# Kernel optimization log

Hardware: AMD Instinct MI355X
Metric: run time of the kernel (lower is better)

Reference implementation:

```python
import jax, jax.numpy as jnp
import numpy as np
from jax.scipy.special import logsumexp

EPS_SINK = 0.1
N_ITERS = 100
LN_EPS = 1e-5
ANAT_W = (1.0, 1.0, 1.2)  # anatomical_weights[0:3] used by _get_region_weights
GRIDS = ((5, 0.2), (15, 0.3), (25, 0.5))  # (grid_size, scale_weight)


def layernorm(x, g, b):
    m = x.mean(-1, keepdims=True)
    v = ((x - m) ** 2).mean(-1, keepdims=True)
    return (x - m) / jnp.sqrt(v + LN_EPS) * g + b


def spatial_distribution(bb, g):
    # bb: [B, D, 4] in 0..1000 coords -> [B, D, g*g] binary occupancy grid
    B, D, _ = bb.shape
    bc = bb * (g / 1000.0)
    x, y, w, h = bc[..., 0], bc[..., 1], bc[..., 2], bc[..., 3]
    x1 = jnp.maximum(jnp.trunc(x), 0.0)          # max(0, int(x))
    y1 = jnp.maximum(jnp.trunc(y), 0.0)
    x2 = jnp.minimum(jnp.trunc(x + w), g - 1.0)  # min(g-1, int(x+w))
    y2 = jnp.minimum(jnp.trunc(y + h), g - 1.0)
    gi = jnp.arange(g, dtype=bb.dtype)
    row = (gi[None, None, :, None] >= y1[..., None, None]) & (gi[None, None, :, None] <= y2[..., None, None])
    col = (gi[None, None, None, :] >= x1[..., None, None]) & (gi[None, None, None, :] <= x2[..., None, None])
    nz = jnp.any(bc != 0, axis=-1)[..., None, None]
    grid = (row & col & nz).astype(bb.dtype)  # [B, D, g, g]
    return grid.reshape(B, D, g * g)


def emd_pairs(d1, d2, g):
    # d1, d2: [B, P, n] spatial distributions; returns [B, P] pseudo-EMD exactly as source
    yy, xx = jnp.meshgrid(jnp.arange(g), jnp.arange(g), indexing='ij')
    pos = jnp.stack([xx.ravel(), yy.ravel()], axis=1).astype(jnp.float32)
    diff = pos[:, None, :] - pos[None, :, :]
    C = jnp.sqrt((diff * diff).sum(-1))
    C = C / C.max()
    rw = jnp.ones((g, g), jnp.float32)
    rw = rw.at[: g // 3].mul(ANAT_W[0]).at[g // 3 : (2 * g) // 3].mul(ANAT_W[1]).at[(2 * g) // 3 :].mul(ANAT_W[2])
    C = C * rw.ravel()  # broadcast over columns, same as torch C[n,n] * weights[n]
    K = jnp.exp(-C / EPS_SINK)
    logP = jnp.log(d1[..., :, None] + 1e-8)  # [B,P,n,1]
    logQ = jnp.log(d2[..., None, :] + 1e-8)  # [B,P,1,n]

    def step(carry, _):
        u, v = carry
        u = logP - logsumexp(v + K, axis=-1, keepdims=True)
        v = logQ - logsumexp(u + K.T, axis=-2, keepdims=True)
        return (u, v), None

    (u, v), _ = jax.lax.scan(step, (jnp.zeros_like(logP), jnp.zeros_like(logQ)), None, length=N_ITERS)
    Pm = jnp.exp(u + v + K)
    return (Pm * C).sum((-2, -1))


def setup_inputs() -> dict:
    key = jax.random.key(0)
    ks = jax.random.split(key, 6)
    B, D, F, Hd = 1, 14, 768, 256
    features = jax.random.normal(ks[0], (B, D, F), jnp.float32)
    # x,y in [0,800), w,h in [0,200) so boxes stay inside the 0..1000 frame
    bb = jax.random.uniform(ks[1], (B, D, 4), jnp.float32) * jnp.array([800.0, 800.0, 200.0, 200.0])
    return {
        'features': features,
        'bb_coords': bb,
        'w_embed': jax.random.normal(ks[2], (F, Hd), jnp.float32) * 0.02,
        'b_embed': jnp.zeros((Hd,), jnp.float32),
        'g1': jnp.ones((Hd,), jnp.float32),
        'b1': jnp.zeros((Hd,), jnp.float32),
        'gat_W': jax.random.normal(ks[3], (3, Hd, Hd), jnp.float32) * 0.02,
        'gat_b': jnp.zeros((3, Hd), jnp.float32),
        'gat_g': jnp.ones((3, Hd), jnp.float32),
        'gat_bt': jnp.zeros((3, Hd), jnp.float32),
        'w_out': jax.random.normal(ks[4], (Hd, F), jnp.float32) * 0.02,
        'b_out': jnp.zeros((F,), jnp.float32),
        'g2': jnp.ones((F,), jnp.float32),
        'b2': jnp.zeros((F,), jnp.float32),
    }


def reference(features, bb_coords, w_embed, b_embed, g1, b1, gat_W, gat_b, gat_g, gat_bt, w_out, b_out, g2, b2):
    B, D, _ = features.shape
    H = 1  # num_heads (the only shape-consistent value for the source module)
    x = layernorm(features @ w_embed + b_embed, g1, b1)

    # --- EMD-based adjacency over all 91 unordered disease pairs, vectorized ---
    iu, ju = np.triu_indices(D, k=1)
    adj = jnp.zeros((B, D, D), features.dtype)
    for g, sw in GRIDS:
        dist = spatial_distribution(bb_coords, g)            # [B, D, g*g]
        emd = emd_pairs(dist[:, iu], dist[:, ju], g)         # [B, 91]
        adj = adj.at[:, iu, ju].add(sw * emd).at[:, ju, iu].add(sw * emd)
    adj = jax.nn.softmax(adj, axis=-1)

    # --- 3 GAT layers (q=k=v, per source) ---
    attns = []
    for l in range(3):
        h = x @ gat_W[l] + gat_b[l]                          # [B, D, 256]
        hd = h.shape[-1] // H
        q = h.reshape(B, D, H, hd).transpose(0, 2, 1, 3)     # [B, H, D, hd]
        attn = jnp.einsum('bhnd,bhmd->bhnm', q, q) * hd ** -0.5
        attn = jnp.where(adj[:, None] == 0, -jnp.inf, attn)
        attn = jax.nn.softmax(attn, axis=-1)
        o = jnp.einsum('bhnm,bhmd->bhnd', attn, q)
        o = o.transpose(0, 2, 1, 3).reshape(B, D, H * hd)
        x = layernorm(o, gat_g[l], gat_bt[l])
        attns.append(attn.mean(1))
        x = jax.nn.elu(x)

    out = layernorm(x @ w_out + b_out, g2, b2)
    final_attention = jnp.stack(attns).mean(0)
    return out, final_attention
```

## Files before the change

### kernel.cpp

```cpp
#include <hip/hip_runtime.h>
#include <math.h>


#define NWG 16

__device__ __forceinline__ void astore(float* p, float v) {
  __hip_atomic_store(p, v, __ATOMIC_RELAXED, __HIP_MEMORY_SCOPE_AGENT);
}

__device__ __forceinline__ void bar_arrive(int* bar, int slot) {
  asm volatile("s_waitcnt vmcnt(0)" ::: "memory");
  __syncthreads();
  if (threadIdx.x == 0)
    __hip_atomic_fetch_add(&bar[slot], 1, __ATOMIC_RELAXED,
                           __HIP_MEMORY_SCOPE_AGENT);
}

__device__ __forceinline__ void bar_wait(int* bar, int slot) {
  if (threadIdx.x == 0) {
    while (__hip_atomic_load(&bar[slot], __ATOMIC_RELAXED,
                             __HIP_MEMORY_SCOPE_AGENT) < NWG)
      __builtin_amdgcn_s_sleep(1);
  }
  __syncthreads();
  asm volatile("" ::: "memory");
}

__device__ __forceinline__ float blockReduce512(float v, float* red) {
#pragma unroll
  for (int off = 32; off; off >>= 1) v += __shfl_xor(v, off);
  __syncthreads();
  if ((threadIdx.x & 63) == 0) red[threadIdx.x >> 6] = v;
  __syncthreads();
  return ((red[0] + red[1]) + (red[2] + red[3])) +
         ((red[4] + red[5]) + (red[6] + red[7]));
}

__device__ __forceinline__ void row_stats(const float* Xs, float* Pb,
                                          float* Mn, float* Rs, int tid) {
  if (tid < 224) {
    const int r = tid >> 4, seg = tid & 15;
    const float* p = Xs + r * 260 + seg * 16;
    const float4 a = *(const float4*)(p);
    const float4 b = *(const float4*)(p + 4);
    const float4 c = *(const float4*)(p + 8);
    const float4 d = *(const float4*)(p + 12);
    Pb[tid] = (((a.x + a.y) + (a.z + a.w)) + ((b.x + b.y) + (b.z + b.w))) +
              (((c.x + c.y) + (c.z + c.w)) + ((d.x + d.y) + (d.z + d.w)));
  }
  __syncthreads();
  if (tid < 14) {
    float s = 0.f;
#pragma unroll
    for (int q = 0; q < 16; ++q) s += Pb[tid * 16 + q];
    Mn[tid] = s * (1.f / 256.f);
  }
  __syncthreads();
  if (tid < 224) {
    const int r = tid >> 4, seg = tid & 15;
    const float m = Mn[r];
    const float* p = Xs + r * 260 + seg * 16;
    float s = 0.f;
#pragma unroll
    for (int i = 0; i < 16; ++i) {
      const float dv = p[i] - m;
      s = fmaf(dv, dv, s);
    }
    Pb[tid] = s;
  }
  __syncthreads();
  if (tid < 14) {
    float s = 0.f;
#pragma unroll
    for (int q = 0; q < 16; ++q) s += Pb[tid * 16 + q];
    Rs[tid] = rsqrtf(s * (1.f / 256.f) + 1e-5f);
  }
  __syncthreads();
}

__global__ __launch_bounds__(512) void sdg_fused(
    const float* __restrict__ feat, const float* __restrict__ w_embed,
    const float* __restrict__ b_embed, const float* __restrict__ g1,
    const float* __restrict__ b1, const float* __restrict__ gat_W,
    const float* __restrict__ gat_b, const float* __restrict__ gat_g,
    const float* __restrict__ gat_bt, const float* __restrict__ w_out,
    const float* __restrict__ b_out, const float* __restrict__ g2,
    const float* __restrict__ b2, float* __restrict__ out, int* bar,
    float* __restrict__ e_ws, float* __restrict__ h_ws,
    float* __restrict__ gp_ws, float* __restrict__ obuf) {
  const int w = blockIdx.x, tid = threadIdx.x;
  const int w16 = w * 16, w48 = w * 48;
  const int c = tid & 15, ks = tid >> 4;

  __shared__ __align__(16) float SA[13056];
  __shared__ __align__(16) float SB[10752];
  __shared__ __align__(16) float Pb[7200];
  __shared__ float Hb[240];
  __shared__ float Asm[224];
  __shared__ float aRow[224];
  __shared__ float Mn[14], Rs[14];
  __shared__ float red8[8];

  float* const Fs = SB;
  float* const Xs = SB;
  float* const Ht = SB + 3640;

#pragma unroll
  for (int i = 0; i < 6; ++i) {
    const int idx = i * 512 + tid;
    const int k = idx >> 2, q = (idx & 3) * 4;
    const float4 v = *(const float4*)(&w_embed[k * 256 + w16 + q]);
    SA[k * 17 + q + 0] = v.x;
    SA[k * 17 + q + 1] = v.y;
    SA[k * 17 + q + 2] = v.z;
    SA[k * 17 + q + 3] = v.w;
  }
  for (int i = tid; i < 2688; i += 512)
    *(float4*)(&Fs[i * 4]) = ((const float4*)feat)[i];
  if (tid < 224) aRow[tid] = 0.f;
  if (tid < 28) Asm[(tid >> 1) * 16 + 14 + (tid & 1)] = 0.f;
  __syncthreads();

  {
    float acc[14];
#pragma unroll
    for (int r = 0; r < 14; ++r) acc[r] = 0.f;
    const int kb = ks * 24;
#pragma unroll
    for (int ch = 0; ch < 6; ++ch) {
      const int k = kb + ch * 4;
      const float w0 = SA[(k + 0) * 17 + c];
      const float w1 = SA[(k + 1) * 17 + c];
      const float w2 = SA[(k + 2) * 17 + c];
      const float w3 = SA[(k + 3) * 17 + c];
#pragma unroll
      for (int r = 0; r < 14; ++r) {
        const float4 xv = *(const float4*)(&Fs[r * 768 + k]);
        acc[r] = fmaf(xv.x, w0,
                      fmaf(xv.y, w1, fmaf(xv.z, w2, fmaf(xv.w, w3, acc[r]))));
      }
    }
#pragma unroll
    for (int r = 0; r < 14; ++r) Pb[ks * 225 + r * 16 + c] = acc[r];
  }
  __syncthreads();
  if (tid < 224) {
    float v = b_embed[w16 + (tid & 15)];
#pragma unroll
    for (int q = 0; q < 32; ++q) v += Pb[q * 225 + tid];
    astore(&e_ws[(tid >> 4) * 256 + w16 + (tid & 15)], v);
  }
  bar_arrive(bar, 0);
#pragma unroll
  for (int i = 0; i < 2; ++i) {
    const int idx = i * 512 + tid;
    const int k = idx >> 2, q = (idx & 3) * 4;
    const float4 v = *(const float4*)(&gat_W[k * 256 + w16 + q]);
    SA[k * 17 + q + 0] = v.x;
    SA[k * 17 + q + 1] = v.y;
    SA[k * 17 + q + 2] = v.z;
    SA[k * 17 + q + 3] = v.w;
  }
  bar_wait(bar, 0);

  for (int i = tid; i < 896; i += 512) {
    const float4 v = ((const float4*)e_ws)[i];
    const int idx = i * 4, r = idx >> 8, cc = idx & 255;
    *(float4*)(&Xs[r * 260 + cc]) = v;
  }
  for (int i = tid; i < 520; i += 512) Ht[14 * 260 + i] = 0.f;
  __syncthreads();
  row_stats(Xs, Pb, Mn, Rs, tid);
  for (int i = tid; i < 3584; i += 512) {
    const int r = i >> 8, cc = i & 255;
    Xs[r * 260 + cc] = (Xs[r * 260 + cc] - Mn[r]) * Rs[r] * g1[cc] + b1[cc];
  }
  __syncthreads();

  for (int l = 0; l < 3; ++l) {
    {
      float acc[14];
#pragma unroll
      for (int r = 0; r < 14; ++r) acc[r] = 0.f;
      const int kb = ks * 8;
#pragma unroll
      for (int ch = 0; ch < 2; ++ch) {
        const int k = kb + ch * 4;
        const float w0 = SA[(k + 0) * 17 + c];
        const float w1 = SA[(k + 1) * 17 + c];
        const float w2 = SA[(k + 2) * 17 + c];
        const float w3 = SA[(k + 3) * 17 + c];
#pragma unroll
        for (int r = 0; r < 14; ++r) {
          const float4 xv = *(const float4*)(&Xs[r * 260 + k]);
          acc[r] = fmaf(
              xv.x, w0, fmaf(xv.y, w1, fmaf(xv.z, w2, fmaf(xv.w, w3, acc[r]))));
        }
      }
#pragma unroll
      for (int r = 0; r < 14; ++r) Pb[ks * 225 + r * 16 + c] = acc[r];
    }
    __syncthreads();
    if (tid < 224) {
      float v = gat_b[l * 256 + w16 + (tid & 15)];
#pragma unroll
      for (int q = 0; q < 32; ++q) v += Pb[q * 225 + tid];
      Hb[(tid >> 4) * 17 + (tid & 15)] = v;
      astore(&h_ws[l * 3584 + (tid >> 4) * 256 + w16 + (tid & 15)], v);
    }
    __syncthreads();
    if (tid < 196) {
      const int i = tid / 14, j = tid - i * 14;
      float s = 0.f;
#pragma unroll
      for (int cc = 0; cc < 16; ++cc)
        s = fmaf(Hb[i * 17 + cc], Hb[j * 17 + cc], s);
      astore(&gp_ws[l * 3328 + w * 208 + tid], s);
    }
    bar_arrive(bar, 1 + l);
    if (l < 2) {
      const float* Wn = gat_W + (l + 1) * 65536;
#pragma unroll
      for (int i = 0; i < 2; ++i) {
        const int idx = i * 512 + tid;
        const int k = idx >> 2, q = (idx & 3) * 4;
        const float4 v = *(const float4*)(&Wn[k * 256 + w16 + q]);
        SA[k * 17 + q + 0] = v.x;
        SA[k * 17 + q + 1] = v.y;
        SA[k * 17 + q + 2] = v.z;
        SA[k * 17 + q + 3] = v.w;
      }
    } else {
#pragma unroll
      for (int g = 0; g < 3; ++g)
#pragma unroll
        for (int i = 0; i < 2; ++i) {
          const int idx = i * 512 + tid;
          const int k = idx >> 2, q = (idx & 3) * 4;
          const float4 v = *(const float4*)(&w_out[k * 768 + w48 + g * 16 + q]);
          SA[g * 4352 + k * 17 + q + 0] = v.x;
          SA[g * 4352 + k * 17 + q + 1] = v.y;
          SA[g * 4352 + k * 17 + q + 2] = v.z;
          SA[g * 4352 + k * 17 + q + 3] = v.w;
        }
    }
    bar_wait(bar, 1 + l);

    float glog = 0.f;
    if (tid < 196) {
      const float* gpl = gp_ws + l * 3328 + tid;
#pragma unroll
      for (int ww = 0; ww < 16; ++ww) glog += gpl[ww * 208];
    }
    for (int i = tid; i < 896; i += 512) {
      const float4 v = ((const float4*)(h_ws + l * 3584))[i];
      const int idx = i * 4, r = idx >> 8, cc = idx & 255;
      *(float4*)(&Ht[r * 260 + cc]) = v;
    }
    if (tid < 196) {
      const int i = tid / 14, j = tid - i * 14;
      Asm[i * 16 + j] = glog * 0.0625f;
    }
    __syncthreads();
    if (tid < 224) {
      const int r = tid >> 4, j = tid & 15;
      const float lv = (j < 14) ? Asm[r * 16 + j] : -1e30f;
      float mx = lv;
#pragma unroll
      for (int off = 8; off; off >>= 1) mx = fmaxf(mx, __shfl_xor(mx, off, 16));
      float p = (j < 14) ? expf(lv - mx) : 0.f;
      float sm = p;
#pragma unroll
      for (int off = 8; off; off >>= 1) sm += __shfl_xor(sm, off, 16);
      p /= sm;
      if (j < 14) {
        Asm[r * 16 + j] = p;
        aRow[r * 16 + j] += p * (1.f / 3.f);
      }
    }
    __syncthreads();
    if (l == 2 && w < 14 && tid < 14)
      out[10752 + w * 14 + tid] = aRow[w * 16 + tid];
    const int half = tid >> 8, t2 = tid & 255;
    float o[7];
#pragma unroll
    for (int rr = 0; rr < 7; ++rr) o[rr] = 0.f;
#pragma unroll
    for (int mc = 0; mc < 4; ++mc) {
      const float v0 = Ht[(mc * 4 + 0) * 260 + t2];
      const float v1 = Ht[(mc * 4 + 1) * 260 + t2];
      const float v2 = Ht[(mc * 4 + 2) * 260 + t2];
      const float v3 = Ht[(mc * 4 + 3) * 260 + t2];
#pragma unroll
      for (int rr = 0; rr < 7; ++rr) {
        const float4 a = *(const float4*)(&Asm[(half * 7 + rr) * 16 + mc * 4]);
        o[rr] =
            fmaf(a.x, v0, fmaf(a.y, v1, fmaf(a.z, v2, fmaf(a.w, v3, o[rr]))));
      }
    }
#pragma unroll
    for (int rr = 0; rr < 7; ++rr) Xs[(half * 7 + rr) * 260 + t2] = o[rr];
    __syncthreads();
    row_stats(Xs, Pb, Mn, Rs, tid);
    {
      const float gc = gat_g[l * 256 + t2], bc = gat_bt[l * 256 + t2];
#pragma unroll
      for (int rr = 0; rr < 7; ++rr) {
        const int r = half * 7 + rr;
        const float xn = (o[rr] - Mn[r]) * Rs[r] * gc + bc;
        Xs[r * 260 + t2] = xn > 0.f ? xn : expm1f(xn);
      }
    }
    __syncthreads();
  }

  for (int g = 0; g < 3; ++g) {
    float acc[14];
#pragma unroll
    for (int r = 0; r < 14; ++r) acc[r] = 0.f;
    const int kb = ks * 8;
#pragma unroll
    for (int ch = 0; ch < 2; ++ch) {
      const int k = kb + ch * 4;
      const float w0 = SA[g * 4352 + (k + 0) * 17 + c];
      const float w1 = SA[g * 4352 + (k + 1) * 17 + c];
      const float w2 = SA[g * 4352 + (k + 2) * 17 + c];
      const float w3 = SA[g * 4352 + (k + 3) * 17 + c];
#pragma unroll
      for (int r = 0; r < 14; ++r) {
        const float4 xv = *(const float4*)(&Xs[r * 260 + k]);
        acc[r] = fmaf(
            xv.x, w0, fmaf(xv.y, w1, fmaf(xv.z, w2, fmaf(xv.w, w3, acc[r]))));
      }
    }
#pragma unroll
    for (int r = 0; r < 14; ++r) Pb[ks * 225 + r * 16 + c] = acc[r];
    __syncthreads();
    if (tid < 224) {
      float v = b_out[w48 + g * 16 + (tid & 15)];
#pragma unroll
      for (int q = 0; q < 32; ++q) v += Pb[q * 225 + tid];
      astore(&obuf[(tid >> 4) * 768 + w48 + g * 16 + (tid & 15)], v);
    }
    __syncthreads();
  }
  bar_arrive(bar, 4);
  bar_wait(bar, 4);

  if (w < 14) {
    const int d = w;
    const float a = obuf[d * 768 + tid];
    const float b = (tid < 256) ? obuf[d * 768 + 512 + tid] : 0.f;
    const float m = blockReduce512(a + b, red8) * (1.f / 768.f);
    const float da = a - m, db = b - m;
    const float var =
        blockReduce512(da * da + ((tid < 256) ? db * db : 0.f), red8) *
        (1.f / 768.f);
    const float rs = rsqrtf(var + 1e-5f);
    out[d * 768 + tid] = da * rs * g2[tid] + b2[tid];
    if (tid < 256)
      out[d * 768 + 512 + tid] = db * rs * g2[512 + tid] + b2[512 + tid];
  }
}

extern "C" void kernel_launch(void* const* d_in, const int* in_sizes, int n_in,
                              void* d_out, int out_size, void* d_ws,
                              size_t ws_size, hipStream_t stream) {
  const float* feat = (const float*)d_in[0];
  const float* w_embed = (const float*)d_in[2];
  const float* b_embed = (const float*)d_in[3];
  const float* g1 = (const float*)d_in[4];
  const float* b1 = (const float*)d_in[5];
  const float* gat_W = (const float*)d_in[6];
  const float* gat_b = (const float*)d_in[7];
  const float* gat_g = (const float*)d_in[8];
  const float* gat_bt = (const float*)d_in[9];
  const float* w_out = (const float*)d_in[10];
  const float* b_out = (const float*)d_in[11];
  const float* g2 = (const float*)d_in[12];
  const float* b2 = (const float*)d_in[13];
  float* out = (float*)d_out;

  int* bar = (int*)d_ws;
  float* e_ws = (float*)d_ws + 16;
  float* h_ws = e_ws + 3584;
  float* gp_ws = h_ws + 3 * 3584;
  float* obuf = gp_ws + 3 * 3328;

  hipMemsetAsync(bar, 0, 16 * sizeof(int), stream);
  sdg_fused<<<NWG, 512, 0, stream>>>(feat, w_embed, b_embed, g1, b1, gat_W,
                                     gat_b, gat_g, gat_bt, w_out, b_out, g2,
                                     b2, out, bar, e_ws, h_ws, gp_ws, obuf);
}
```

Baseline: 42.42 us.

## Double block size and compute layernorm stats via partial sums across workgroups

```diff
diff --git a/kernel.cpp b/kernel.cpp
--- a/kernel.cpp
+++ b/kernel.cpp
@@ -24,16 +24,6 @@
   }
   __syncthreads();
   asm volatile("" ::: "memory");
-}
-
-__device__ __forceinline__ float blockReduce512(float v, float* red) {
-#pragma unroll
-  for (int off = 32; off; off >>= 1) v += __shfl_xor(v, off);
-  __syncthreads();
-  if ((threadIdx.x & 63) == 0) red[threadIdx.x >> 6] = v;
-  __syncthreads();
-  return ((red[0] + red[1]) + (red[2] + red[3])) +
-         ((red[4] + red[5]) + (red[6] + red[7]));
 }
 
 __device__ __forceinline__ void row_stats(const float* Xs, float* Pb,
@@ -78,7 +68,7 @@
   __syncthreads();
 }
 
-__global__ __launch_bounds__(512) void sdg_fused(
+__global__ __launch_bounds__(1024) void sdg_fused(
     const float* __restrict__ feat, const float* __restrict__ w_embed,
     const float* __restrict__ b_embed, const float* __restrict__ g1,
     const float* __restrict__ b1, const float* __restrict__ gat_W,
@@ -87,91 +77,120 @@
     const float* __restrict__ b_out, const float* __restrict__ g2,
     const float* __restrict__ b2, float* __restrict__ out, int* bar,
     float* __restrict__ e_ws, float* __restrict__ h_ws,
-    float* __restrict__ gp_ws, float* __restrict__ obuf) {
+    float* __restrict__ gp_ws, float* __restrict__ st1_ws,
+    float* __restrict__ st2_ws) {
   const int w = blockIdx.x, tid = threadIdx.x;
   const int w16 = w * 16, w48 = w * 48;
-  const int c = tid & 15, ks = tid >> 4;
-
-  __shared__ __align__(16) float SA[13056];
+  const int c = tid & 15;
+  const int ksl = (tid >> 4) & 15;
+  const int rg = tid >> 8;
+
+  __shared__ __align__(16) float SA[14592];
   __shared__ __align__(16) float SB[10752];
-  __shared__ __align__(16) float Pb[7200];
+  __shared__ __align__(16) float Pb[3600];
   __shared__ float Hb[240];
   __shared__ float Asm[224];
   __shared__ float aRow[224];
-  __shared__ float Mn[14], Rs[14];
-  __shared__ float red8[8];
+  __shared__ float Ov[686];
+  __shared__ float Mn[14], Rs[14], ps[14], psq[14];
 
   float* const Fs = SB;
   float* const Xs = SB;
   float* const Ht = SB + 3640;
 
 #pragma unroll
-  for (int i = 0; i < 6; ++i) {
-    const int idx = i * 512 + tid;
+  for (int i = 0; i < 3; ++i) {
+    const int idx = i * 1024 + tid;
     const int k = idx >> 2, q = (idx & 3) * 4;
     const float4 v = *(const float4*)(&w_embed[k * 256 + w16 + q]);
-    SA[k * 17 + q + 0] = v.x;
-    SA[k * 17 + q + 1] = v.y;
-    SA[k * 17 + q + 2] = v.z;
-    SA[k * 17 + q + 3] = v.w;
-  }
-  for (int i = tid; i < 2688; i += 512)
+    SA[k * 19 + q + 0] = v.x;
+    SA[k * 19 + q + 1] = v.y;
+    SA[k * 19 + q + 2] = v.z;
+    SA[k * 19 + q + 3] = v.w;
+  }
+  for (int i = tid; i < 2688; i += 1024)
     *(float4*)(&Fs[i * 4]) = ((const float4*)feat)[i];
   if (tid < 224) aRow[tid] = 0.f;
   if (tid < 28) Asm[(tid >> 1) * 16 + 14 + (tid & 1)] = 0.f;
   __syncthreads();
 
   {
-    float acc[14];
-#pragma unroll
-    for (int r = 0; r < 14; ++r) acc[r] = 0.f;
-    const int kb = ks * 24;
-#pragma unroll
-    for (int ch = 0; ch < 6; ++ch) {
+    float acc[4] = {0.f, 0.f, 0.f, 0.f};
+    const int r0 = rg * 4, kb = ksl * 48;
+#pragma unroll
+    for (int ch = 0; ch < 12; ++ch) {
       const int k = kb + ch * 4;
-      const float w0 = SA[(k + 0) * 17 + c];
-      const float w1 = SA[(k + 1) * 17 + c];
-      const float w2 = SA[(k + 2) * 17 + c];
-      const float w3 = SA[(k + 3) * 17 + c];
-#pragma unroll
-      for (int r = 0; r < 14; ++r) {
-        const float4 xv = *(const float4*)(&Fs[r * 768 + k]);
-        acc[r] = fmaf(xv.x, w0,
-                      fmaf(xv.y, w1, fmaf(xv.z, w2, fmaf(xv.w, w3, acc[r]))));
-      }
-    }
-#pragma unroll
-    for (int r = 0; r < 14; ++r) Pb[ks * 225 + r * 16 + c] = acc[r];
+      const float w0 = SA[(k + 0) * 19 + c];
+      const float w1 = SA[(k + 1) * 19 + c];
+      const float w2 = SA[(k + 2) * 19 + c];
+      const float w3 = SA[(k + 3) * 19 + c];
+#pragma unroll
+      for (int rr = 0; rr < 4; ++rr) {
+        const int r = r0 + rr;
+        if (r < 14) {
+          const float4 xv = *(const float4*)(&Fs[r * 768 + k]);
+          acc[rr] = fmaf(
+              xv.x, w0,
+              fmaf(xv.y, w1, fmaf(xv.z, w2, fmaf(xv.w, w3, acc[rr]))));
+        }
+      }
+    }
+#pragma unroll
+    for (int rr = 0; rr < 4; ++rr) {
+      const int r = r0 + rr;
+      if (r < 14) Pb[ksl * 225 + r * 16 + c] = acc[rr];
+    }
   }
   __syncthreads();
   if (tid < 224) {
-    float v = b_embed[w16 + (tid & 15)];
-#pragma unroll
-    for (int q = 0; q < 32; ++q) v += Pb[q * 225 + tid];
-    astore(&e_ws[(tid >> 4) * 256 + w16 + (tid & 15)], v);
+    const int r = tid >> 4, cc = tid & 15;
+    float v = b_embed[w16 + cc];
+#pragma unroll
+    for (int q = 0; q < 16; ++q) v += Pb[q * 225 + tid];
+    astore(&e_ws[r * 256 + w16 + cc], v);
+    float sv = v, sq = v * v;
+#pragma unroll
+    for (int off = 8; off; off >>= 1) {
+      sv += __shfl_xor(sv, off, 16);
+      sq += __shfl_xor(sq, off, 16);
+    }
+    if (cc == 0) {
+      astore(&st1_ws[w * 28 + r], sv);
+      astore(&st1_ws[w * 28 + 14 + r], sq);
+    }
   }
   bar_arrive(bar, 0);
-#pragma unroll
-  for (int i = 0; i < 2; ++i) {
-    const int idx = i * 512 + tid;
-    const int k = idx >> 2, q = (idx & 3) * 4;
+  {
+    const int k = tid >> 2, q = (tid & 3) * 4;
     const float4 v = *(const float4*)(&gat_W[k * 256 + w16 + q]);
-    SA[k * 17 + q + 0] = v.x;
-    SA[k * 17 + q + 1] = v.y;
-    SA[k * 17 + q + 2] = v.z;
-    SA[k * 17 + q + 3] = v.w;
+    SA[k * 19 + q + 0] = v.x;
+    SA[k * 19 + q + 1] = v.y;
+    SA[k * 19 + q + 2] = v.z;
+    SA[k * 19 + q + 3] = v.w;
   }
   bar_wait(bar, 0);
 
-  for (int i = tid; i < 896; i += 512) {
-    const float4 v = ((const float4*)e_ws)[i];
-    const int idx = i * 4, r = idx >> 8, cc = idx & 255;
+  if (tid < 14) {
+    float S = 0.f, Q = 0.f;
+#pragma unroll
+    for (int q = 0; q < 16; ++q) {
+      S += st1_ws[q * 28 + tid];
+      Q += st1_ws[q * 28 + 14 + tid];
+    }
+    const float m = S * (1.f / 256.f);
+    Mn[tid] = m;
+    Rs[tid] = rsqrtf(Q * (1.f / 256.f) - m * m + 1e-5f);
+    ps[tid] = 0.f;
+    psq[tid] = 0.f;
+  }
+  if (tid < 896) {
+    const float4 v = ((const float4*)e_ws)[tid];
+    const int idx = tid * 4, r = idx >> 8, cc = idx & 255;
     *(float4*)(&Xs[r * 260 + cc]) = v;
   }
-  for (int i = tid; i < 520; i += 512) Ht[14 * 260 + i] = 0.f;
-  __syncthreads();
-  row_stats(Xs, Pb, Mn, Rs, tid);
-  for (int i = tid; i < 3584; i += 512) {
+  if (tid < 520) Ht[14 * 260 + tid] = 0.f;
+  __syncthreads();
+  for (int i = tid; i < 3584; i += 1024) {
     const int r = i >> 8, cc = i & 255;
     Xs[r * 260 + cc] = (Xs[r * 260 + cc] - Mn[r]) * Rs[r] * g1[cc] + b1[cc];
   }
@@ -179,34 +198,40 @@
 
   for (int l = 0; l < 3; ++l) {
     {
-      float acc[14];
-#pragma unroll
-      for (int r = 0; r < 14; ++r) acc[r] = 0.f;
-      const int kb = ks * 8;
-#pragma unroll
-      for (int ch = 0; ch < 2; ++ch) {
+      float acc[4] = {0.f, 0.f, 0.f, 0.f};
+      const int r0 = rg * 4, kb = ksl * 16;
+#pragma unroll
+      for (int ch = 0; ch < 4; ++ch) {
         const int k = kb + ch * 4;
-        const float w0 = SA[(k + 0) * 17 + c];
-        const float w1 = SA[(k + 1) * 17 + c];
-        const float w2 = SA[(k + 2) * 17 + c];
-        const float w3 = SA[(k + 3) * 17 + c];
-#pragma unroll
-        for (int r = 0; r < 14; ++r) {
-          const float4 xv = *(const float4*)(&Xs[r * 260 + k]);
-          acc[r] = fmaf(
-              xv.x, w0, fmaf(xv.y, w1, fmaf(xv.z, w2, fmaf(xv.w, w3, acc[r]))));
+        const float w0 = SA[(k + 0) * 19 + c];
+        const float w1 = SA[(k + 1) * 19 + c];
+        const float w2 = SA[(k + 2) * 19 + c];
+        const float w3 = SA[(k + 3) * 19 + c];
+#pragma unroll
+        for (int rr = 0; rr < 4; ++rr) {
+          const int r = r0 + rr;
+          if (r < 14) {
+            const float4 xv = *(const float4*)(&Xs[r * 260 + k]);
+            acc[rr] = fmaf(
+                xv.x, w0,
+                fmaf(xv.y, w1, fmaf(xv.z, w2, fmaf(xv.w, w3, acc[rr]))));
+          }
         }
       }
 #pragma unroll
-      for (int r = 0; r < 14; ++r) Pb[ks * 225 + r * 16 + c] = acc[r];
+      for (int rr = 0; rr < 4; ++rr) {
+        const int r = r0 + rr;
+        if (r < 14) Pb[ksl * 225 + r * 16 + c] = acc[rr];
+      }
     }
     __syncthreads();
     if (tid < 224) {
-      float v = gat_b[l * 256 + w16 + (tid & 15)];
-#pragma unroll
-      for (int q = 0; q < 32; ++q) v += Pb[q * 225 + tid];
-      Hb[(tid >> 4) * 17 + (tid & 15)] = v;
-      astore(&h_ws[l * 3584 + (tid >> 4) * 256 + w16 + (tid & 15)], v);
+      const int r = tid >> 4, cc = tid & 15;
+      float v = gat_b[l * 256 + w16 + cc];
+#pragma unroll
+      for (int q = 0; q < 16; ++q) v += Pb[q * 225 + tid];
+      Hb[r * 17 + cc] = v;
+      astore(&h_ws[l * 3584 + r * 256 + w16 + cc], v);
     }
     __syncthreads();
     if (tid < 196) {
@@ -220,29 +245,22 @@
     bar_arrive(bar, 1 + l);
     if (l < 2) {
       const float* Wn = gat_W + (l + 1) * 65536;
-#pragma unroll
-      for (int i = 0; i < 2; ++i) {
-        const int idx = i * 512 + tid;
-        const int k = idx >> 2, q = (idx & 3) * 4;
-        const float4 v = *(const float4*)(&Wn[k * 256 + w16 + q]);
-        SA[k * 17 + q + 0] = v.x;
-        SA[k * 17 + q + 1] = v.y;
-        SA[k * 17 + q + 2] = v.z;
-        SA[k * 17 + q + 3] = v.w;
-      }
+      const int k = tid >> 2, q = (tid & 3) * 4;
+      const float4 v = *(const float4*)(&Wn[k * 256 + w16 + q]);
+      SA[k * 19 + q + 0] = v.x;
+      SA[k * 19 + q + 1] = v.y;
+      SA[k * 19 + q + 2] = v.z;
+      SA[k * 19 + q + 3] = v.w;
     } else {
 #pragma unroll
-      for (int g = 0; g < 3; ++g)
-#pragma unroll
-        for (int i = 0; i < 2; ++i) {
-          const int idx = i * 512 + tid;
-          const int k = idx >> 2, q = (idx & 3) * 4;
-          const float4 v = *(const float4*)(&w_out[k * 768 + w48 + g * 16 + q]);
-          SA[g * 4352 + k * 17 + q + 0] = v.x;
-          SA[g * 4352 + k * 17 + q + 1] = v.y;
-          SA[g * 4352 + k * 17 + q + 2] = v.z;
-          SA[g * 4352 + k * 17 + q + 3] = v.w;
-        }
+      for (int g = 0; g < 3; ++g) {
+        const int k = tid >> 2, q = (tid & 3) * 4;
+        const float4 v = *(const float4*)(&w_out[k * 768 + w48 + g * 16 + q]);
+        SA[g * 4864 + k * 19 + q + 0] = v.x;
+        SA[g * 4864 + k * 19 + q + 1] = v.y;
+        SA[g * 4864 + k * 19 + q + 2] = v.z;
+        SA[g * 4864 + k * 19 + q + 3] = v.w;
+      }
     }
     bar_wait(bar, 1 + l);
 
@@ -252,9 +270,9 @@
 #pragma unroll
       for (int ww = 0; ww < 16; ++ww) glog += gpl[ww * 208];
     }
-    for (int i = tid; i < 896; i += 512) {
-      const float4 v = ((const float4*)(h_ws + l * 3584))[i];
-      const int idx = i * 4, r = idx >> 8, cc = idx & 255;
+    if (tid < 896) {
+      const float4 v = ((const float4*)(h_ws + l * 3584))[tid];
+      const int idx = tid * 4, r = idx >> 8, cc = idx & 255;
       *(float4*)(&Ht[r * 260 + cc]) = v;
     }
     if (tid < 196) {
@@ -281,10 +299,8 @@
     __syncthreads();
     if (l == 2 && w < 14 && tid < 14)
       out[10752 + w * 14 + tid] = aRow[w * 16 + tid];
-    const int half = tid >> 8, t2 = tid & 255;
-    float o[7];
-#pragma unroll
-    for (int rr = 0; rr < 7; ++rr) o[rr] = 0.f;
+    const int t2 = tid & 255;
+    float o[4] = {0.f, 0.f, 0.f, 0.f};
 #pragma unroll
     for (int mc = 0; mc < 4; ++mc) {
       const float v0 = Ht[(mc * 4 + 0) * 260 + t2];
@@ -292,74 +308,111 @@
       const float v2 = Ht[(mc * 4 + 2) * 260 + t2];
       const float v3 = Ht[(mc * 4 + 3) * 260 + t2];
 #pragma unroll
-      for (int rr = 0; rr < 7; ++rr) {
-        const float4 a = *(const float4*)(&Asm[(half * 7 + rr) * 16 + mc * 4]);
-        o[rr] =
-            fmaf(a.x, v0, fmaf(a.y, v1, fmaf(a.z, v2, fmaf(a.w, v3, o[rr]))));
-      }
-    }
-#pragma unroll
-    for (int rr = 0; rr < 7; ++rr) Xs[(half * 7 + rr) * 260 + t2] = o[rr];
+      for (int rr = 0; rr < 4; ++rr) {
+        const int r = rg * 4 + rr;
+        if (r < 14) {
+          const float4 a = *(const float4*)(&Asm[r * 16 + mc * 4]);
+          o[rr] =
+              fmaf(a.x, v0, fmaf(a.y, v1, fmaf(a.z, v2, fmaf(a.w, v3, o[rr]))));
+        }
+      }
+    }
+#pragma unroll
+    for (int rr = 0; rr < 4; ++rr) {
+      const int r = rg * 4 + rr;
+      if (r < 14) Xs[r * 260 + t2] = o[rr];
+    }
     __syncthreads();
     row_stats(Xs, Pb, Mn, Rs, tid);
     {
       const float gc = gat_g[l * 256 + t2], bc = gat_bt[l * 256 + t2];
 #pragma unroll
-      for (int rr = 0; rr < 7; ++rr) {
-        const int r = half * 7 + rr;
-        const float xn = (o[rr] - Mn[r]) * Rs[r] * gc + bc;
-        Xs[r * 260 + t2] = xn > 0.f ? xn : expm1f(xn);
+      for (int rr = 0; rr < 4; ++rr) {
+        const int r = rg * 4 + rr;
+        if (r < 14) {
+          const float xn = (o[rr] - Mn[r]) * Rs[r] * gc + bc;
+          Xs[r * 260 + t2] = xn > 0.f ? xn : expm1f(xn);
+        }
       }
     }
     __syncthreads();
   }
 
   for (int g = 0; g < 3; ++g) {
-    float acc[14];
-#pragma unroll
-    for (int r = 0; r < 14; ++r) acc[r] = 0.f;
-    const int kb = ks * 8;
-#pragma unroll
-    for (int ch = 0; ch < 2; ++ch) {
-      const int k = kb + ch * 4;
-      const float w0 = SA[g * 4352 + (k + 0) * 17 + c];
-      const float w1 = SA[g * 4352 + (k + 1) * 17 + c];
-      const float w2 = SA[g * 4352 + (k + 2) * 17 + c];
-      const float w3 = SA[g * 4352 + (k + 3) * 17 + c];
-#pragma unroll
-      for (int r = 0; r < 14; ++r) {
-        const float4 xv = *(const float4*)(&Xs[r * 260 + k]);
-        acc[r] = fmaf(
-            xv.x, w0, fmaf(xv.y, w1, fmaf(xv.z, w2, fmaf(xv.w, w3, acc[r]))));
-      }
-    }
-#pragma unroll
-    for (int r = 0; r < 14; ++r) Pb[ks * 225 + r * 16 + c] = acc[r];
+    {
+      float acc[4] = {0.f, 0.f, 0.f, 0.f};
+      const int r0 = rg * 4, kb = ksl * 16;
+#pragma unroll
+      for (int ch = 0; ch < 4; ++ch) {
+        const int k = kb + ch * 4;
+        const float w0 = SA[g * 4864 + (k + 0) * 19 + c];
+        const float w1 = SA[g * 4864 + (k + 1) * 19 + c];
+        const float w2 = SA[g * 4864 + (k + 2) * 19 + c];
+        const float w3 = SA[g * 4864 + (k + 3) * 19 + c];
+#pragma unroll
+        for (int rr = 0; rr < 4; ++rr) {
+          const int r = r0 + rr;
+          if (r < 14) {
+            const float4 xv = *(const float4*)(&Xs[r * 260 + k]);
+            acc[rr] = fmaf(
+                xv.x, w0,
+                fmaf(xv.y, w1, fmaf(xv.z, w2, fmaf(xv.w, w3, acc[rr]))));
+          }
+        }
+      }
+#pragma unroll
+      for (int rr = 0; rr < 4; ++rr) {
+        const int r = r0 + rr;
+        if (r < 14) Pb[ksl * 225 + r * 16 + c] = acc[rr];
+      }
+    }
     __syncthreads();
     if (tid < 224) {
-      float v = b_out[w48 + g * 16 + (tid & 15)];
-#pragma unroll
-      for (int q = 0; q < 32; ++q) v += Pb[q * 225 + tid];
-      astore(&obuf[(tid >> 4) * 768 + w48 + g * 16 + (tid & 15)], v);
-    }
-    __syncthreads();
+      const int r = tid >> 4, cc = tid & 15;
+      float v = b_out[w48 + g * 16 + cc];
+#pragma unroll
+      for (int q = 0; q < 16; ++q) v += Pb[q * 225 + tid];
+      Ov[r * 49 + g * 16 + cc] = v;
+      float sv = v, sq = v * v;
+#pragma unroll
+      for (int off = 8; off; off >>= 1) {
+        sv += __shfl_xor(sv, off, 16);
+        sq += __shfl_xor(sq, off, 16);
+      }
+      if (cc == 0) {
+        ps[r] += sv;
+        psq[r] += sq;
+      }
+    }
+    __syncthreads();
+  }
+  if (tid < 14) {
+    astore(&st2_ws[w * 28 + tid], ps[tid]);
+    astore(&st2_ws[w * 28 + 14 + tid], psq[tid]);
   }
   bar_arrive(bar, 4);
   bar_wait(bar, 4);
-
-  if (w < 14) {
-    const int d = w;
-    const float a = obuf[d * 768 + tid];
-    const float b = (tid < 256) ? obuf[d * 768 + 512 + tid] : 0.f;
-    const float m = blockReduce512(a + b, red8) * (1.f / 768.f);
-    const float da = a - m, db = b - m;
-    const float var =
-        blockReduce512(da * da + ((tid < 256) ? db * db : 0.f), red8) *
-        (1.f / 768.f);
-    const float rs = rsqrtf(var + 1e-5f);
-    out[d * 768 + tid] = da * rs * g2[tid] + b2[tid];
-    if (tid < 256)
-      out[d * 768 + 512 + tid] = db * rs * g2[512 + tid] + b2[512 + tid];
+  if (tid < 14) {
+    float S = 0.f, Q = 0.f;
+#pragma unroll
+    for (int q = 0; q < 16; ++q) {
+      S += st2_ws[q * 28 + tid];
+      Q += st2_ws[q * 28 + 14 + tid];
+    }
+    const float m = S * (1.f / 768.f);
+    Mn[tid] = m;
+    Rs[tid] = rsqrtf(Q * (1.f / 768.f) - m * m + 1e-5f);
+  }
+  __syncthreads();
+  if (tid < 224) {
+    const int r = tid >> 4, cc = tid & 15;
+    const float m = Mn[r], rs = Rs[r];
+#pragma unroll
+    for (int g = 0; g < 3; ++g) {
+      const int col = w48 + g * 16 + cc;
+      out[r * 768 + col] = (Ov[r * 49 + g * 16 + cc] - m) * rs * g2[col] +
+                           b2[col];
+    }
   }
 }
 
@@ -385,10 +438,12 @@
   float* e_ws = (float*)d_ws + 16;
   float* h_ws = e_ws + 3584;
   float* gp_ws = h_ws + 3 * 3584;
-  float* obuf = gp_ws + 3 * 3328;
+  float* st1_ws = gp_ws + 3 * 3328;
+  float* st2_ws = st1_ws + 448;
 
   hipMemsetAsync(bar, 0, 16 * sizeof(int), stream);
-  sdg_fused<<<NWG, 512, 0, stream>>>(feat, w_embed, b_embed, g1, b1, gat_W,
-                                     gat_b, gat_g, gat_bt, w_out, b_out, g2,
-                                     b2, out, bar, e_ws, h_ws, gp_ws, obuf);
-}
+  sdg_fused<<<NWG, 1024, 0, stream>>>(feat, w_embed, b_embed, g1, b1, gat_W,
+                                      gat_b, gat_g, gat_bt, w_out, b_out, g2,
+                                      b2, out, bar, e_ws, h_ws, gp_ws, st1_ws,
+                                      st2_ws);
+}
```

Result: faster. 40.62 us (-4.2%).
